# Kernel optimization log

Measured on AMD Instinct MI355X. Metric: run time of the kernel, lower is better.

Reference implementation:

```python
import jax, jax.numpy as jnp
import numpy as np

N, OBS, ENC, ACT, K = 16384, 512, 512, 64, 8
ALPHA = 1.0


def setup_inputs() -> dict:
    key = jax.random.key(0)
    ks = jax.random.split(key, 8)
    s = 0.05  # keep activations/logits well-scaled
    return {
        "X1": jax.random.normal(ks[0], (N, OBS), jnp.float32),
        "X0": jax.random.normal(ks[1], (N, OBS), jnp.float32),
        "U": jax.random.normal(ks[2], (N, ACT), jnp.float32),
        "W_enc": jax.random.normal(ks[3], (ENC, OBS), jnp.float32) * s,
        "A_all": jax.random.normal(ks[4], (K, ENC, ENC), jnp.float32) * s,
        "B_rest": jax.random.normal(ks[5], (K - 1, ACT, ENC), jnp.float32) * s,
        "C_w": jax.random.normal(ks[6], (K, ENC), jnp.float32) * s,
        "C_b": jax.random.normal(ks[7], (K,), jnp.float32) * s,
    }


def reference(X1, X0, U, W_enc, A_all, B_rest, C_w, C_b):
    enc_dim = W_enc.shape[0]
    act_dim = U.shape[1]
    k = A_all.shape[0]
    # encoder: bias-free linear
    X1e = X1 @ W_enc.T  # [N, enc]
    X0e = X0 @ W_enc.T  # [N, enc]
    # gating: argmax of linear classifier C
    inds = jnp.argmax(X0e @ C_w.T + C_b, axis=1)  # [N]
    # expert 0 uses fixed B0 = eye(enc)[:act, :]; experts 1..k-1 learned
    B0 = jnp.eye(enc_dim, dtype=X0.dtype)[:act_dim]  # [act, enc]
    B_all = jnp.concatenate([B0[None], B_rest], axis=0)  # [k, act, enc]
    # per-expert predictions for every row (nn.Linear: x @ W.T -> einsum over input dim h)
    preds = jnp.einsum('nh,keh->kne', X0e, A_all) + jnp.einsum('na,kae->kne', U, B_all)
    # squared error per (expert, row), then select each row's routed expert
    sq = jnp.sum((X1e[None, :, :] - preds) ** 2, axis=-1)  # [k, N]
    onehot = jax.nn.one_hot(inds, k, dtype=sq.dtype)  # [N, k]
    loss = ALPHA * jnp.sum(sq * onehot.T)
    return loss / (enc_dim * X1.shape[0])
```

## Files before the change

### kernel.cpp

```cpp
#include <hip/hip_runtime.h>

#define NROWS 16384
#define OBSD 512
#define ENCD 512
#define ACTD 64
#define KEXP 8

typedef __attribute__((ext_vector_type(8))) short bf16x8;
typedef __attribute__((ext_vector_type(4))) float f32x4;
typedef __attribute__((address_space(3))) unsigned char lds_byte;
typedef __attribute__((address_space(1))) unsigned char glb_byte;

__device__ __forceinline__ unsigned short f2bf(float f) {
  unsigned int u = __float_as_uint(f);
  u = (u + 0x7FFFu + ((u >> 16) & 1u)) >> 16;
  return (unsigned short)u;
}
__device__ __forceinline__ unsigned int cvtpk(float lo, float hi) {
  unsigned int r;
  asm("v_cvt_pk_bf16_f32 %0, %1, %2" : "=v"(r) : "v"(lo), "v"(hi));
  return r;
}
__device__ __forceinline__ void gload_lds16(const unsigned short* g, unsigned short* l) {
  __builtin_amdgcn_global_load_lds((const glb_byte*)g, (lds_byte*)l, 16, 0, 0);
}

__global__ __launch_bounds__(256) void gt_k(
    const float* __restrict__ W, const float* __restrict__ Cw,
    float* __restrict__ GT, float* __restrict__ loss,
    int* __restrict__ counts, int* __restrict__ cursor) {
  const int b = blockIdx.x, tid = threadIdx.x;
  if (b == 0) {
    if (tid == 0) *loss = 0.f;
    if (tid < KEXP) { counts[tid] = 0; cursor[tid] = 0; }
  }
  __shared__ float red[4][64];
  int e = b >> 3, o0 = (b & 7) * 64;
  int o = tid & 63, hg = tid >> 6;
  float s = 0.f;
#pragma unroll 8
  for (int h = hg * 128; h < hg * 128 + 128; h++)
    s += Cw[e * ENCD + h] * W[(size_t)h * OBSD + o0 + o];
  red[hg][o] = s;
  __syncthreads();
  if (tid < 64)
    GT[(o0 + tid) * KEXP + e] = red[0][tid] + red[1][tid] + red[2][tid] + red[3][tid];
}

__global__ __launch_bounds__(256) void fused_prep_k(
    const float* __restrict__ X0, const float* __restrict__ X1,
    const float* __restrict__ U, const float* __restrict__ W,
    const float* __restrict__ Aall, const float* __restrict__ Brest,
    const float* __restrict__ GT, const float* __restrict__ Cb,
    unsigned short* __restrict__ X0bf, unsigned short* __restrict__ X1bf,
    unsigned short* __restrict__ Ubf, unsigned short* __restrict__ Wbf,
    unsigned short* __restrict__ AbfN, unsigned short* __restrict__ BfTN,
    unsigned short* __restrict__ WbfT, int* __restrict__ inds,
    int* __restrict__ counts) {
  const int b = blockIdx.x, tid = threadIdx.x;
  if (b < 512) {
    __shared__ int lhist[KEXP];
    if (tid < KEXP) lhist[tid] = 0;
    __syncthreads();
    const int lane = tid & 63, w = tid >> 6;
    float g[8][8];
    const float* gp = GT + lane * 8 * KEXP;
#pragma unroll
    for (int j = 0; j < 8; j++) {
      float4 lo = *(const float4*)(gp + j * KEXP);
      float4 hi = *(const float4*)(gp + j * KEXP + 4);
      g[j][0] = lo.x; g[j][1] = lo.y; g[j][2] = lo.z; g[j][3] = lo.w;
      g[j][4] = hi.x; g[j][5] = hi.y; g[j][6] = hi.z; g[j][7] = hi.w;
    }
    float cb[KEXP];
#pragma unroll
    for (int e = 0; e < KEXP; e++) cb[e] = Cb[e];
#pragma unroll 2
    for (int r = 0; r < 8; r++) {
      const int n = b * 32 + w * 8 + r;
      const float4* xr = (const float4*)(X0 + (size_t)n * OBSD + lane * 8);
      float4 x = xr[0], y = xr[1];
      float xv[8] = {x.x, x.y, x.z, x.w, y.x, y.y, y.z, y.w};
      float acc[KEXP] = {};
#pragma unroll
      for (int j = 0; j < 8; j++)
#pragma unroll
        for (int e = 0; e < KEXP; e++) acc[e] += xv[j] * g[j][e];
      uint4 rr = {cvtpk(x.x, x.y), cvtpk(x.z, x.w), cvtpk(y.x, y.y), cvtpk(y.z, y.w)};
      *(uint4*)&X0bf[(size_t)n * OBSD + lane * 8] = rr;
#pragma unroll
      for (int e = 0; e < KEXP; e++) {
#pragma unroll
        for (int off = 32; off > 0; off >>= 1) acc[e] += __shfl_xor(acc[e], off, 64);
      }
      if (lane == 0) {
        int best = 0;
        float bv = acc[0] + cb[0];
#pragma unroll
        for (int e = 1; e < KEXP; e++) {
          float v = acc[e] + cb[e];
          if (v > bv) { bv = v; best = e; }
        }
        inds[n] = best;
        atomicAdd(&lhist[best], 1);
      }
    }
    __syncthreads();
    if (tid < KEXP) atomicAdd(&counts[tid], lhist[tid]);
    return;
  }
  if (b < 4608) {
    size_t i = ((size_t)(b - 512) * 256 + tid) * 8;
    const float4* s4 = (const float4*)(X1 + i);
    float4 a = s4[0], c = s4[1];
    uint4 r = {cvtpk(a.x, a.y), cvtpk(a.z, a.w), cvtpk(c.x, c.y), cvtpk(c.z, c.w)};
    *(uint4*)&X1bf[i] = r;
    return;
  }
  if (b < 4664) {
    __shared__ float tile[64][65];
    int t = b - 4608;
    int k = (t >> 3);
    int e0 = (t & 7) * 64;
    const float* src = Brest + (size_t)k * ACTD * ENCD + e0;
#pragma unroll
    for (int j = 0; j < 16; j++) {
      int idx = j * 256 + tid;
      int a = idx >> 6, e = idx & 63;
      tile[a][e] = src[(size_t)a * ENCD + e];
    }
    __syncthreads();
    unsigned short* dst = BfTN + ((size_t)(k + 1) * ENCD + e0) * ACTD;
#pragma unroll
    for (int j = 0; j < 16; j++) {
      int idx = j * 256 + tid;
      int e = idx >> 6, a = idx & 63;
      dst[(size_t)e * ACTD + a] = f2bf(-tile[a][e]);
    }
    return;
  }
  if (b == 4664) {
    for (int j = 0; j < 16; j++) {
      int i8 = j * 256 + tid;
      int e = i8 >> 3, a0 = (i8 & 7) * 8;
      unsigned int w0 = 0, w1 = 0, w2 = 0, w3 = 0;
      if (e >= a0 && e < a0 + 8) {
        unsigned int bits = 0xBF80u << ((e & 1) * 16);
        if ((e - a0) >> 1 == 0) w0 = bits;
        else if ((e - a0) >> 1 == 1) w1 = bits;
        else if ((e - a0) >> 1 == 2) w2 = bits;
        else w3 = bits;
      }
      uint4 v = {w0, w1, w2, w3};
      *(uint4*)&BfTN[(size_t)i8 * 8] = v;
    }
    return;
  }
  if (b < 7993) {
    int cb2 = b - 4665;
    if (cb2 < 1024) {
      size_t i = (size_t)cb2 * 256 + tid;
      float4 v = ((const float4*)U)[i];
      uint2 r = {cvtpk(v.x, v.y), cvtpk(v.z, v.w)};
      *(uint2*)&Ubf[i * 4] = r;
    } else if (cb2 < 1280) {
      size_t i = (size_t)(cb2 - 1024) * 256 + tid;
      float4 v = ((const float4*)W)[i];
      uint2 r = {cvtpk(v.x, v.y), cvtpk(v.z, v.w)};
      *(uint2*)&Wbf[i * 4] = r;
    } else {
      size_t i = (size_t)(cb2 - 1280) * 256 + tid;
      float4 v = ((const float4*)Aall)[i];
      uint2 r = {cvtpk(-v.x, -v.y), cvtpk(-v.z, -v.w)};
      *(uint2*)&AbfN[i * 4] = r;
    }
    return;
  }
  {
    __shared__ float tile[64][65];
    int t = b - 7993;
    int h0 = (t >> 3) * 64, o0 = (t & 7) * 64;
#pragma unroll
    for (int j = 0; j < 16; j++) {
      int idx = j * 256 + tid;
      int a = idx >> 6, e = idx & 63;
      tile[a][e] = W[(size_t)(h0 + a) * OBSD + o0 + e];
    }
    __syncthreads();
#pragma unroll
    for (int j = 0; j < 16; j++) {
      int idx = j * 256 + tid;
      int e = idx >> 6, a = idx & 63;
      WbfT[(size_t)(o0 + e) * OBSD + h0 + a] = f2bf(tile[a][e]);
    }
  }
}

__global__ __launch_bounds__(256, 2) void scatmgemm_k(
    const int* __restrict__ inds, const int* __restrict__ counts,
    int* __restrict__ cursor, int* __restrict__ rowlist,
    const unsigned short* __restrict__ AbfN, const unsigned short* __restrict__ WbfT,
    unsigned short* __restrict__ MN) {
  if (blockIdx.x < 64) {
    __shared__ int lhist[KEXP], lbase[KEXP], sstart[KEXP];
    const int tid = threadIdx.x;
    if (tid < KEXP) {
      lhist[tid] = 0;
      int s = 0;
      for (int j = 0; j < KEXP; j++) {
        if (j == tid) sstart[tid] = s;
        s += counts[j];
      }
    }
    __syncthreads();
    const int n = blockIdx.x * 256 + tid;
    const int r = inds[n];
    const int lpos = atomicAdd(&lhist[r], 1);
    __syncthreads();
    if (tid < KEXP) lbase[tid] = atomicAdd(&cursor[tid], lhist[tid]);
    __syncthreads();
    rowlist[sstart[r] + lbase[r] + lpos] = n;
    return;
  }
  __shared__ unsigned short As[128 * 64];
  __shared__ unsigned short Bs[128 * 64];
  const int tid = threadIdx.x;
  const int t = blockIdx.x - 64;
  const int k = t >> 4;
  const int rem = t & 15;
  const int row0 = (rem >> 2) * 128;
  const int col0 = (rem & 3) * 128;

  const int lane = tid & 63, w = tid >> 6;
  const int wr = w >> 1, wc = w & 1;
  const int srow8 = tid >> 3;
  const int lslot = ((tid & 7) ^ (srow8 & 7)) * 8;
  const int ldsoff = tid * 8;
  const int r15 = lane & 15;
  const int qk = lane >> 4;
  const int rsw = r15 & 7;
  const int arow = wr * 64 + r15;
  const int brow = wc * 64 + r15;
  const unsigned short* Ak = AbfN + (size_t)k * ENCD * ENCD;

  f32x4 acc[4][4] = {};
  for (int k0 = 0; k0 < ENCD; k0 += 64) {
#pragma unroll
    for (int j = 0; j < 4; j++) {
      int row = j * 32 + srow8;
      gload_lds16(Ak + (size_t)(row0 + row) * ENCD + k0 + lslot, &As[j * 2048 + ldsoff]);
      gload_lds16(WbfT + (size_t)(col0 + row) * OBSD + k0 + lslot, &Bs[j * 2048 + ldsoff]);
    }
    __syncthreads();
#pragma unroll
    for (int kk = 0; kk < 2; kk++) {
      const int ps = ((kk * 4 + qk) ^ rsw) * 8;
      bf16x8 af[4], bfr[4];
#pragma unroll
      for (int m = 0; m < 4; m++) af[m] = *(const bf16x8*)&As[(arow + m * 16) * 64 + ps];
#pragma unroll
      for (int n = 0; n < 4; n++) bfr[n] = *(const bf16x8*)&Bs[(brow + n * 16) * 64 + ps];
#pragma unroll
      for (int m = 0; m < 4; m++)
#pragma unroll
        for (int n = 0; n < 4; n++)
          acc[m][n] = __builtin_amdgcn_mfma_f32_16x16x32_bf16(bfr[n], af[m], acc[m][n], 0, 0, 0);
    }
    __syncthreads();
  }
  unsigned short* Mk = MN + (size_t)k * ENCD * OBSD;
#pragma unroll
  for (int m = 0; m < 4; m++) {
    int rowg = row0 + wr * 64 + m * 16 + r15;
#pragma unroll
    for (int n = 0; n < 4; n++) {
      int colg = col0 + wc * 64 + n * 16 + qk * 4;
      uint2 v = {cvtpk(acc[m][n][0], acc[m][n][1]), cvtpk(acc[m][n][2], acc[m][n][3])};
      *(uint2*)&Mk[(size_t)rowg * OBSD + colg] = v;
    }
  }
}

__global__ __launch_bounds__(256, 2) void grouped_mfma_k(
    const unsigned short* __restrict__ X1bf, const unsigned short* __restrict__ X0bf,
    const unsigned short* __restrict__ Wbf, const unsigned short* __restrict__ Ubf,
    const unsigned short* __restrict__ MN, const unsigned short* __restrict__ BfTN,
    const int* __restrict__ rowlist, const int* __restrict__ counts,
    float* __restrict__ loss) {
  const int tid = threadIdx.x;
  const int bid = blockIdx.x;
  const int lid = (bid & 7) * 512 + (bid >> 3);
  const int k = lid >> 9;
  const int rem = lid & 511;
  const int col0 = (rem & 3) * 128;
  const int tile = rem >> 2;

  int start = 0, cnt = 0;
#pragma unroll
  for (int j = 0; j < KEXP; j++) {
    int c = counts[j];
    if (j < k) start += c;
    if (j == k) cnt = c;
  }
  if (tile * 128 >= cnt) return;

  __shared__ unsigned short As[128 * 64];
  __shared__ unsigned short Bs[128 * 64];
  __shared__ int ridx[128];
  __shared__ float red[4];

  if (tid < 128) {
    int p = tile * 128 + tid;
    ridx[tid] = rowlist[start + (p < cnt ? p : 0)];
  }
  __syncthreads();

  const int lane = tid & 63, w = tid >> 6;
  const int wr = w >> 1, wc = w & 1;
  const int srow8 = tid >> 3;
  const int lslot = ((tid & 7) ^ (srow8 & 7)) * 8;
  const int ldsoff = tid * 8;
  const int r15 = lane & 15;
  const int qk = lane >> 4;
  const int rsw = r15 & 7;
  const int arow = wr * 64 + r15;
  const int brow = wc * 64 + r15;
  int rnj[4];
#pragma unroll
  for (int j = 0; j < 4; j++) rnj[j] = ridx[j * 32 + srow8];

  const unsigned short* MkN = MN + (size_t)k * ENCD * OBSD;
  const unsigned short* BfTkN = BfTN + (size_t)k * ENCD * ACTD;

  f32x4 acc[4][4] = {};
#define GROUPED_COMPUTE()                                                            \
  do {                                                                               \
    __syncthreads();                                                                 \
    _Pragma("unroll") for (int kk = 0; kk < 2; kk++) {                               \
      const int ps = ((kk * 4 + qk) ^ rsw) * 8;                                      \
      bf16x8 af[4], bfr[4];                                                          \
      _Pragma("unroll") for (int m = 0; m < 4; m++)                                  \
          af[m] = *(const bf16x8*)&As[(arow + m * 16) * 64 + ps];                    \
      _Pragma("unroll") for (int n = 0; n < 4; n++)                                  \
          bfr[n] = *(const bf16x8*)&Bs[(brow + n * 16) * 64 + ps];                   \
      _Pragma("unroll") for (int m = 0; m < 4; m++)                                  \
          _Pragma("unroll") for (int n = 0; n < 4; n++)                              \
              acc[m][n] = __builtin_amdgcn_mfma_f32_16x16x32_bf16(bfr[n], af[m],     \
                                                                  acc[m][n], 0, 0, 0); \
    }                                                                                \
    __syncthreads();                                                                 \
  } while (0)

  for (int k0 = 0; k0 < OBSD; k0 += 64) {
#pragma unroll
    for (int j = 0; j < 4; j++) {
      int row = j * 32 + srow8;
      gload_lds16(X1bf + (size_t)rnj[j] * OBSD + k0 + lslot, &As[j * 2048 + ldsoff]);
      gload_lds16(Wbf + (size_t)(col0 + row) * OBSD + k0 + lslot, &Bs[j * 2048 + ldsoff]);
    }
    GROUPED_COMPUTE();
  }
  for (int k0 = 0; k0 < OBSD; k0 += 64) {
#pragma unroll
    for (int j = 0; j < 4; j++) {
      int row = j * 32 + srow8;
      gload_lds16(X0bf + (size_t)rnj[j] * OBSD + k0 + lslot, &As[j * 2048 + ldsoff]);
      gload_lds16(MkN + (size_t)(col0 + row) * OBSD + k0 + lslot, &Bs[j * 2048 + ldsoff]);
    }
    GROUPED_COMPUTE();
  }
  {
#pragma unroll
    for (int j = 0; j < 4; j++) {
      int row = j * 32 + srow8;
      gload_lds16(Ubf + (size_t)rnj[j] * ACTD + lslot, &As[j * 2048 + ldsoff]);
      gload_lds16(BfTkN + (size_t)(col0 + row) * ACTD + lslot, &Bs[j * 2048 + ldsoff]);
    }
    GROUPED_COMPUTE();
  }
#undef GROUPED_COMPUTE

  float sq = 0.f;
#pragma unroll
  for (int m = 0; m < 4; m++) {
    int lr = wr * 64 + m * 16 + r15;
    if (tile * 128 + lr < cnt) {
#pragma unroll
      for (int n = 0; n < 4; n++)
        sq += acc[m][n][0] * acc[m][n][0] + acc[m][n][1] * acc[m][n][1] +
              acc[m][n][2] * acc[m][n][2] + acc[m][n][3] * acc[m][n][3];
    }
  }
#pragma unroll
  for (int off = 32; off > 0; off >>= 1) sq += __shfl_xor(sq, off, 64);
  if (lane == 0) red[w] = sq;
  __syncthreads();
  if (tid == 0) atomicAdd(loss, red[0] + red[1] + red[2] + red[3]);
}

__global__ void finalize_k(const float* __restrict__ loss, float* __restrict__ out) {
  if (threadIdx.x == 0 && blockIdx.x == 0)
    out[0] = loss[0] * (1.0f / ((float)ENCD * (float)NROWS));
}

extern "C" void kernel_launch(void* const* d_in, const int* in_sizes, int n_in,
                              void* d_out, int out_size, void* d_ws, size_t ws_size,
                              hipStream_t stream) {
  const float* X1 = (const float*)d_in[0];
  const float* X0 = (const float*)d_in[1];
  const float* U = (const float*)d_in[2];
  const float* W = (const float*)d_in[3];
  const float* Aall = (const float*)d_in[4];
  const float* Brest = (const float*)d_in[5];
  const float* Cw = (const float*)d_in[6];
  const float* Cb = (const float*)d_in[7];
  float* out = (float*)d_out;

  char* p = (char*)d_ws;
  auto alloc = [&](size_t bytes) { char* r = p; p += (bytes + 255) & ~(size_t)255; return r; };
  unsigned short* X1bf = (unsigned short*)alloc((size_t)NROWS * OBSD * 2);
  unsigned short* X0bf = (unsigned short*)alloc((size_t)NROWS * OBSD * 2);
  unsigned short* Ubf = (unsigned short*)alloc((size_t)NROWS * ACTD * 2);
  unsigned short* Wbf = (unsigned short*)alloc((size_t)ENCD * OBSD * 2);
  unsigned short* AbfN = (unsigned short*)alloc((size_t)KEXP * ENCD * ENCD * 2);
  unsigned short* BfTN = (unsigned short*)alloc((size_t)KEXP * ENCD * ACTD * 2);
  unsigned short* WbfT = (unsigned short*)alloc((size_t)OBSD * ENCD * 2);
  unsigned short* MN = (unsigned short*)alloc((size_t)KEXP * ENCD * OBSD * 2);
  float* GT = (float*)alloc(KEXP * OBSD * 4);
  float* loss = (float*)alloc(256);
  int* inds = (int*)alloc(NROWS * 4);
  int* rowlist = (int*)alloc(NROWS * 4);
  int* counts = (int*)alloc(64);
  int* cursor = (int*)alloc(64);

  gt_k<<<64, 256, 0, stream>>>(W, Cw, GT, loss, counts, cursor);
  fused_prep_k<<<8057, 256, 0, stream>>>(X0, X1, U, W, Aall, Brest, GT, Cb,
                                         X0bf, X1bf, Ubf, Wbf, AbfN, BfTN,
                                         WbfT, inds, counts);
  scatmgemm_k<<<192, 256, 0, stream>>>(inds, counts, cursor, rowlist,
                                       AbfN, WbfT, MN);
  grouped_mfma_k<<<4096, 256, 0, stream>>>(X1bf, X0bf, Wbf, Ubf, MN, BfTN,
                                           rowlist, counts, loss);
  finalize_k<<<1, 64, 0, stream>>>(loss, out);
}
```

Before: 79.07 us.

## Fuse A fp32-to-bf16 negation into the M GEMM and raise grouped occupancy

Removes the separate pass in the prep kernel that converted and negated A_all into a bf16 workspace buffer. The scatmgemm kernel now loads fp32 A directly, converts it in registers and writes it to swizzled LDS, with the K tile shrunk from 64 to 32. This saves a full write and re-read of the 8x512x512 bf16 A buffer and about 2000 prep blocks. The cost is more loop iterations and barriers in the GEMM and fp32 loads that are twice as large. Separately, the launch bounds of grouped_mfma_k are raised to 4 blocks per SM, which may force register spilling.

```diff
diff --git a/kernel.cpp b/kernel.cpp
--- a/kernel.cpp
+++ b/kernel.cpp
@@ -50,13 +50,12 @@
 __global__ __launch_bounds__(256) void fused_prep_k(
     const float* __restrict__ X0, const float* __restrict__ X1,
     const float* __restrict__ U, const float* __restrict__ W,
-    const float* __restrict__ Aall, const float* __restrict__ Brest,
-    const float* __restrict__ GT, const float* __restrict__ Cb,
+    const float* __restrict__ Brest, const float* __restrict__ GT,
+    const float* __restrict__ Cb,
     unsigned short* __restrict__ X0bf, unsigned short* __restrict__ X1bf,
     unsigned short* __restrict__ Ubf, unsigned short* __restrict__ Wbf,
-    unsigned short* __restrict__ AbfN, unsigned short* __restrict__ BfTN,
-    unsigned short* __restrict__ WbfT, int* __restrict__ inds,
-    int* __restrict__ counts) {
+    unsigned short* __restrict__ BfTN, unsigned short* __restrict__ WbfT,
+    int* __restrict__ inds, int* __restrict__ counts) {
   const int b = blockIdx.x, tid = threadIdx.x;
   if (b < 512) {
     __shared__ int lhist[KEXP];
@@ -156,29 +155,24 @@
     }
     return;
   }
-  if (b < 7993) {
+  if (b < 5945) {
     int cb2 = b - 4665;
     if (cb2 < 1024) {
       size_t i = (size_t)cb2 * 256 + tid;
       float4 v = ((const float4*)U)[i];
       uint2 r = {cvtpk(v.x, v.y), cvtpk(v.z, v.w)};
       *(uint2*)&Ubf[i * 4] = r;
-    } else if (cb2 < 1280) {
+    } else {
       size_t i = (size_t)(cb2 - 1024) * 256 + tid;
       float4 v = ((const float4*)W)[i];
       uint2 r = {cvtpk(v.x, v.y), cvtpk(v.z, v.w)};
       *(uint2*)&Wbf[i * 4] = r;
-    } else {
-      size_t i = (size_t)(cb2 - 1280) * 256 + tid;
-      float4 v = ((const float4*)Aall)[i];
-      uint2 r = {cvtpk(-v.x, -v.y), cvtpk(-v.z, -v.w)};
-      *(uint2*)&AbfN[i * 4] = r;
     }
     return;
   }
   {
     __shared__ float tile[64][65];
-    int t = b - 7993;
+    int t = b - 5945;
     int h0 = (t >> 3) * 64, o0 = (t & 7) * 64;
 #pragma unroll
     for (int j = 0; j < 16; j++) {
@@ -199,7 +193,7 @@
 __global__ __launch_bounds__(256, 2) void scatmgemm_k(
     const int* __restrict__ inds, const int* __restrict__ counts,
     int* __restrict__ cursor, int* __restrict__ rowlist,
-    const unsigned short* __restrict__ AbfN, const unsigned short* __restrict__ WbfT,
+    const float* __restrict__ Aall, const unsigned short* __restrict__ WbfT,
     unsigned short* __restrict__ MN) {
   if (blockIdx.x < 64) {
     __shared__ int lhist[KEXP], lbase[KEXP], sstart[KEXP];
@@ -222,8 +216,8 @@
     rowlist[sstart[r] + lbase[r] + lpos] = n;
     return;
   }
-  __shared__ unsigned short As[128 * 64];
-  __shared__ unsigned short Bs[128 * 64];
+  __shared__ unsigned short As[128 * 32];
+  __shared__ unsigned short Bs[128 * 32];
   const int tid = threadIdx.x;
   const int t = blockIdx.x - 64;
   const int k = t >> 4;
@@ -233,55 +227,59 @@
 
   const int lane = tid & 63, w = tid >> 6;
   const int wr = w >> 1, wc = w & 1;
-  const int srow8 = tid >> 3;
-  const int lslot = ((tid & 7) ^ (srow8 & 7)) * 8;
+  const int srow = tid >> 1, sj = tid & 1;
+  const int swz = (srow >> 1) & 3;
+  const int wo0 = srow * 32 + ((2 * sj) ^ swz) * 8;
+  const int wo1 = srow * 32 + ((2 * sj + 1) ^ swz) * 8;
+  const int gslot = ((tid & 3) ^ ((tid >> 3) & 3)) * 8;
+  const int srowB = tid >> 2;
   const int ldsoff = tid * 8;
-  const int r15 = lane & 15;
-  const int qk = lane >> 4;
-  const int rsw = r15 & 7;
-  const int arow = wr * 64 + r15;
-  const int brow = wc * 64 + r15;
-  const unsigned short* Ak = AbfN + (size_t)k * ENCD * ENCD;
+  const int rslot = ((lane >> 4) ^ (((lane & 15) >> 1) & 3)) * 8;
+  const int arow = wr * 64 + (lane & 15);
+  const int brow = wc * 64 + (lane & 15);
+  const float* pA = Aall + ((size_t)k * ENCD + row0 + srow) * ENCD + sj * 16;
 
   f32x4 acc[4][4] = {};
-  for (int k0 = 0; k0 < ENCD; k0 += 64) {
-#pragma unroll
-    for (int j = 0; j < 4; j++) {
-      int row = j * 32 + srow8;
-      gload_lds16(Ak + (size_t)(row0 + row) * ENCD + k0 + lslot, &As[j * 2048 + ldsoff]);
-      gload_lds16(WbfT + (size_t)(col0 + row) * OBSD + k0 + lslot, &Bs[j * 2048 + ldsoff]);
-    }
-    __syncthreads();
-#pragma unroll
-    for (int kk = 0; kk < 2; kk++) {
-      const int ps = ((kk * 4 + qk) ^ rsw) * 8;
-      bf16x8 af[4], bfr[4];
-#pragma unroll
-      for (int m = 0; m < 4; m++) af[m] = *(const bf16x8*)&As[(arow + m * 16) * 64 + ps];
-#pragma unroll
-      for (int n = 0; n < 4; n++) bfr[n] = *(const bf16x8*)&Bs[(brow + n * 16) * 64 + ps];
-#pragma unroll
-      for (int m = 0; m < 4; m++)
-#pragma unroll
-        for (int n = 0; n < 4; n++)
-          acc[m][n] = __builtin_amdgcn_mfma_f32_16x16x32_bf16(bfr[n], af[m], acc[m][n], 0, 0, 0);
-    }
+  for (int k0 = 0; k0 < ENCD; k0 += 32) {
+    float4 a0 = *(const float4*)(pA + k0);
+    float4 a1 = *(const float4*)(pA + k0 + 4);
+    float4 a2 = *(const float4*)(pA + k0 + 8);
+    float4 a3 = *(const float4*)(pA + k0 + 12);
+    uint4 pa0 = {cvtpk(-a0.x, -a0.y), cvtpk(-a0.z, -a0.w),
+                 cvtpk(-a1.x, -a1.y), cvtpk(-a1.z, -a1.w)};
+    uint4 pa1 = {cvtpk(-a2.x, -a2.y), cvtpk(-a2.z, -a2.w),
+                 cvtpk(-a3.x, -a3.y), cvtpk(-a3.z, -a3.w)};
+    *(uint4*)&As[wo0] = pa0;
+    *(uint4*)&As[wo1] = pa1;
+    gload_lds16(WbfT + (size_t)(col0 + srowB) * OBSD + k0 + gslot, &Bs[ldsoff]);
+    gload_lds16(WbfT + (size_t)(col0 + 64 + srowB) * OBSD + k0 + gslot, &Bs[2048 + ldsoff]);
+    __syncthreads();
+    bf16x8 af[4], bfr[4];
+#pragma unroll
+    for (int m = 0; m < 4; m++) af[m] = *(const bf16x8*)&As[(arow + m * 16) * 32 + rslot];
+#pragma unroll
+    for (int n = 0; n < 4; n++) bfr[n] = *(const bf16x8*)&Bs[(brow + n * 16) * 32 + rslot];
+#pragma unroll
+    for (int m = 0; m < 4; m++)
+#pragma unroll
+      for (int n = 0; n < 4; n++)
+        acc[m][n] = __builtin_amdgcn_mfma_f32_16x16x32_bf16(bfr[n], af[m], acc[m][n], 0, 0, 0);
     __syncthreads();
   }
   unsigned short* Mk = MN + (size_t)k * ENCD * OBSD;
 #pragma unroll
   for (int m = 0; m < 4; m++) {
-    int rowg = row0 + wr * 64 + m * 16 + r15;
+    int rowg = row0 + wr * 64 + m * 16 + (lane & 15);
 #pragma unroll
     for (int n = 0; n < 4; n++) {
-      int colg = col0 + wc * 64 + n * 16 + qk * 4;
+      int colg = col0 + wc * 64 + n * 16 + (lane >> 4) * 4;
       uint2 v = {cvtpk(acc[m][n][0], acc[m][n][1]), cvtpk(acc[m][n][2], acc[m][n][3])};
       *(uint2*)&Mk[(size_t)rowg * OBSD + colg] = v;
     }
   }
 }
 
-__global__ __launch_bounds__(256, 2) void grouped_mfma_k(
+__global__ __launch_bounds__(256, 4) void grouped_mfma_k(
     const unsigned short* __restrict__ X1bf, const unsigned short* __restrict__ X0bf,
     const unsigned short* __restrict__ Wbf, const unsigned short* __restrict__ Ubf,
     const unsigned short* __restrict__ MN, const unsigned short* __restrict__ BfTN,
@@ -422,7 +420,6 @@
   unsigned short* X0bf = (unsigned short*)alloc((size_t)NROWS * OBSD * 2);
   unsigned short* Ubf = (unsigned short*)alloc((size_t)NROWS * ACTD * 2);
   unsigned short* Wbf = (unsigned short*)alloc((size_t)ENCD * OBSD * 2);
-  unsigned short* AbfN = (unsigned short*)alloc((size_t)KEXP * ENCD * ENCD * 2);
   unsigned short* BfTN = (unsigned short*)alloc((size_t)KEXP * ENCD * ACTD * 2);
   unsigned short* WbfT = (unsigned short*)alloc((size_t)OBSD * ENCD * 2);
   unsigned short* MN = (unsigned short*)alloc((size_t)KEXP * ENCD * OBSD * 2);
@@ -434,11 +431,11 @@
   int* cursor = (int*)alloc(64);
 
   gt_k<<<64, 256, 0, stream>>>(W, Cw, GT, loss, counts, cursor);
-  fused_prep_k<<<8057, 256, 0, stream>>>(X0, X1, U, W, Aall, Brest, GT, Cb,
-                                         X0bf, X1bf, Ubf, Wbf, AbfN, BfTN,
-                                         WbfT, inds, counts);
+  fused_prep_k<<<6009, 256, 0, stream>>>(X0, X1, U, W, Brest, GT, Cb,
+                                         X0bf, X1bf, Ubf, Wbf, BfTN, WbfT,
+                                         inds, counts);
   scatmgemm_k<<<192, 256, 0, stream>>>(inds, counts, cursor, rowlist,
-                                       AbfN, WbfT, MN);
+                                       Aall, WbfT, MN);
   grouped_mfma_k<<<4096, 256, 0, stream>>>(X1bf, X0bf, Wbf, Ubf, MN, BfTN,
                                            rowlist, counts, loss);
   finalize_k<<<1, 64, 0, stream>>>(loss, out);
```

Measured after the change: 86.55 us. 9.5% more time.
